# Performance work log

Measured on AMD Instinct MI355X. Metric: run time of the kernel, lower is better.

The kernel has to match this reference:

```python
import jax, jax.numpy as jnp
import numpy as np
import math

B, S, D, H = 4, 1024, 1024, 16

def setup_inputs() -> dict:
    key = jax.random.key(0)
    ks = jax.random.split(key, 9)
    Q = jax.random.normal(ks[0], (B, S, D), dtype=jnp.float32)
    K = jax.random.normal(ks[1], (B, S, D), dtype=jnp.float32)
    V = jax.random.normal(ks[2], (B, S, D), dtype=jnp.float32)
    mask = jax.random.randint(ks[3], (B, 1, S, S), 0, 2, dtype=jnp.int32)
    # keep the diagonal unmasked so no causal row is fully -inf (avoids NaN softmax rows)
    eye = jnp.eye(S, dtype=jnp.int32)[None, None]
    mask = jnp.maximum(mask, eye)
    sc = 1.0 / math.sqrt(D)
    Wq = jax.random.normal(ks[4], (D, D), dtype=jnp.float32) * sc
    Wk = jax.random.normal(ks[5], (D, D), dtype=jnp.float32) * sc
    Wv = jax.random.normal(ks[6], (D, D), dtype=jnp.float32) * sc
    Wo = jax.random.normal(ks[7], (D, D), dtype=jnp.float32) * sc
    bo = jnp.zeros((D,), dtype=jnp.float32)
    return {"Q": Q, "K": K, "V": V, "mask": mask,
            "Wq": Wq, "Wk": Wk, "Wv": Wv, "Wo": Wo, "bo": bo, "heads": H}


def reference(Q, K, V, mask, Wq, Wk, Wv, Wo, bo, heads):
    b, s, d = Q.shape
    dk = d // heads
    # QKV projections (bias-free) and head split: [B,S,D] -> [B,H,S,dk]
    def split_heads(x, W):
        return (x @ W).reshape(b, s, heads, dk).transpose(0, 2, 1, 3)
    q = split_heads(Q, Wq)
    k = split_heads(K, Wk)
    v = split_heads(V, Wv)
    # raw scores [B,H,S,S]
    attn = jnp.einsum('bhqd,bhkd->bhqk', q, k) / jnp.sqrt(jnp.float32(dk))
    # multiplicative padding mask
    attn = attn * mask.astype(attn.dtype)
    # sequential=True: torch.tril zeroes the strict upper triangle
    causal = jnp.tril(jnp.ones((s, s), dtype=attn.dtype))
    attn = attn * causal
    # the module's quirk: exact zeros become -inf before softmax
    attn = jnp.where(attn == 0, -jnp.inf, attn)
    scores = jax.nn.softmax(attn, axis=-1)  # dropout is identity in eval / p=0
    ctx = jnp.einsum('bhqk,bhkd->bhqd', scores, v)
    concat = ctx.transpose(0, 2, 1, 3).reshape(b, s, d)
    return concat @ Wo + bo
```

## Files before the change

### kernel.cpp

```cpp
#include <hip/hip_runtime.h>

#define DEV __device__ __forceinline__

typedef __bf16 bf16x8 __attribute__((ext_vector_type(8)));
typedef float f32x4 __attribute__((ext_vector_type(4)));
typedef unsigned short u16x8 __attribute__((ext_vector_type(8)));
typedef unsigned int u32;
typedef unsigned long long u64;

DEV unsigned short f2bf(float f) {
  union { float f; unsigned int u; } v; v.f = f;
  unsigned int r = v.u + 0x7fffu + ((v.u >> 16) & 1u);
  return (unsigned short)(r >> 16);
}

DEV int swz(int row, int kbyte) { return row * 128 + (kbyte ^ ((row & 7) << 4)); }

DEV void gload16(const void* g, void* l) {
  __builtin_amdgcn_global_load_lds(
      (const __attribute__((address_space(1))) unsigned int*)g,
      (__attribute__((address_space(3))) unsigned int*)l, 16, 0, 0);
}

__global__ __launch_bounds__(256) void prep_k(
    const int* __restrict__ mask, u32* __restrict__ bits,
    const float* __restrict__ Qx, const float* __restrict__ Kx, const float* __restrict__ Vx,
    unsigned short* __restrict__ qp, unsigned short* __restrict__ kp,
    unsigned short* __restrict__ vp,
    const float* __restrict__ W0, const float* __restrict__ W1,
    const float* __restrict__ W2, const float* __restrict__ W3,
    unsigned short* __restrict__ O0, unsigned short* __restrict__ O1,
    unsigned short* __restrict__ O2, unsigned short* __restrict__ O3) {
  __shared__ float tile[32][33];
  int bid = blockIdx.x, t = threadIdx.x;
  if (bid < 16384) {
    int e = bid * 256 + t;
    int k = e & 1023, q = (e >> 10) & 1023;
    int m = (mask[e] != 0) && (k <= q);
    unsigned long long b = __ballot(m);
    int lane = t & 63;
    if (lane == 0)       bits[e >> 5] = (u32)b;
    else if (lane == 32) bits[e >> 5] = (u32)(b >> 32);
  } else if (bid < 17920) {
    int r2 = bid - 16384;
    int z = r2 >> 9, tl = r2 & 511;
    const float* X = z == 0 ? Qx : z == 1 ? Kx : Vx;
    unsigned short* P = z == 0 ? qp : z == 1 ? kp : vp;
    int mb = tl >> 4, kt = tl & 15;
    size_t tb = (size_t)tl * 16384;
    #pragma unroll
    for (int i = 0; i < 4; i++) {
      int idx = i * 256 + t;
      int r = idx >> 3, j = idx & 7;
      int c0 = ((j * 16) ^ ((r & 7) << 4)) >> 1;
      const float* src = X + (size_t)(mb * 128 + r) * 1024 + kt * 64 + c0;
      f32x4 a = *(const f32x4*)src;
      f32x4 bq = *(const f32x4*)(src + 4);
      u16x8 o;
      o[0] = f2bf(a[0]); o[1] = f2bf(a[1]); o[2] = f2bf(a[2]); o[3] = f2bf(a[3]);
      o[4] = f2bf(bq[0]); o[5] = f2bf(bq[1]); o[6] = f2bf(bq[2]); o[7] = f2bf(bq[3]);
      *(u16x8*)((char*)P + tb + (size_t)idx * 16) = o;
    }
  } else {
    int r2 = bid - 17920;
    int z = r2 >> 10, rem = r2 & 1023;
    const float* W = z == 0 ? W0 : z == 1 ? W1 : z == 2 ? W2 : W3;
    unsigned short* O = z == 0 ? O0 : z == 1 ? O1 : z == 2 ? O2 : O3;
    int tx = t & 31, ty = t >> 5;
    int x0 = (rem & 31) * 32, y0 = (rem >> 5) * 32;
    #pragma unroll
    for (int i = 0; i < 4; i++)
      tile[ty + i * 8][tx] = W[(size_t)(y0 + ty + i * 8) * 1024 + x0 + tx];
    __syncthreads();
    #pragma unroll
    for (int i = 0; i < 4; i++) {
      int n = x0 + ty + i * 8, k = y0 + tx;
      size_t a = (size_t)((n >> 7) * 16 + (k >> 6)) * 16384 + swz(n & 127, (k & 63) * 2);
      *(unsigned short*)((char*)O + a) = f2bf(tile[tx][ty + i * 8]);
    }
  }
}

__global__ __launch_bounds__(256) void proj_gemm_k(
    const unsigned short* __restrict__ Qp, const unsigned short* __restrict__ Kp,
    const unsigned short* __restrict__ Vp,
    const unsigned short* __restrict__ Wtq, const unsigned short* __restrict__ Wtk,
    const unsigned short* __restrict__ Wtv,
    unsigned short* __restrict__ qo, unsigned short* __restrict__ ko,
    unsigned short* __restrict__ vo) {
  int z = blockIdx.z;
  const unsigned short* Ap = z == 0 ? Qp : z == 1 ? Kp : Vp;
  const unsigned short* Bp = z == 0 ? Wtq : z == 1 ? Wtk : Wtv;
  unsigned short* out = z == 0 ? qo : z == 1 ? ko : vo;

  __shared__ __align__(16) unsigned short As[8192];
  __shared__ __align__(16) unsigned short Bs[8192];

  int t = threadIdx.x, w = t >> 6, lane = t & 63;
  int wm = (w >> 1) * 64, wn = (w & 1) * 64;
  int rl = lane & 15, kgrp = lane >> 4;

  f32x4 acc[4][4];
  #pragma unroll
  for (int m = 0; m < 4; m++)
    #pragma unroll
    for (int n = 0; n < 4; n++)
      #pragma unroll
      for (int r = 0; r < 4; r++) acc[m][n][r] = 0.f;

  for (int kt = 0; kt < 16; kt++) {
    __syncthreads();
    const char* ab = (const char*)Ap + (size_t)(blockIdx.x * 16 + kt) * 16384 + w * 1024 + lane * 16;
    const char* bb = (const char*)Bp + (size_t)(blockIdx.y * 16 + kt) * 16384 + w * 1024 + lane * 16;
    char* al = (char*)As + w * 1024;
    char* bl = (char*)Bs + w * 1024;
    #pragma unroll
    for (int i = 0; i < 4; i++) {
      gload16(ab + i * 4096, al + i * 4096);
      gload16(bb + i * 4096, bl + i * 4096);
    }
    __syncthreads();
    #pragma unroll
    for (int kk = 0; kk < 2; kk++) {
      bf16x8 af[4], bfr[4];
      #pragma unroll
      for (int m = 0; m < 4; m++)
        af[m] = *(const bf16x8*)((const char*)As + swz(wm + m * 16 + rl, kk * 64 + kgrp * 16));
      #pragma unroll
      for (int n = 0; n < 4; n++)
        bfr[n] = *(const bf16x8*)((const char*)Bs + swz(wn + n * 16 + rl, kk * 64 + kgrp * 16));
      #pragma unroll
      for (int m = 0; m < 4; m++)
        #pragma unroll
        for (int n = 0; n < 4; n++)
          acc[m][n] = __builtin_amdgcn_mfma_f32_16x16x32_bf16(af[m], bfr[n], acc[m][n], 0, 0, 0);
    }
  }
  int m0 = blockIdx.x * 128, n0 = blockIdx.y * 128;
  #pragma unroll
  for (int m = 0; m < 4; m++)
    #pragma unroll
    for (int n = 0; n < 4; n++)
      #pragma unroll
      for (int r = 0; r < 4; r++) {
        int grow = m0 + wm + m * 16 + kgrp * 4 + r;
        int gcol = n0 + wn + n * 16 + rl;
        int b = grow >> 10, s = grow & 1023;
        int h = gcol >> 6, d = gcol & 63;
        unsigned short val = f2bf(acc[m][n][r]);
        if (z == 0) {
          out[(size_t)((b * 16 + h) * 1024 + s) * 64 + d] = val;
        } else if (z == 1) {
          *(unsigned short*)((char*)out +
            (size_t)((b * 16 + h) * 16 + (s >> 6)) * 8192 + swz(s & 63, d * 2)) = val;
        } else {
          *(unsigned short*)((char*)out +
            (size_t)((b * 16 + h) * 16 + (s >> 6)) * 8192 + swz(d, (s & 63) * 2)) = val;
        }
      }
}

__global__ __launch_bounds__(256) void attn_k(
    const unsigned short* __restrict__ qg, const unsigned short* __restrict__ kp,
    const unsigned short* __restrict__ vp, const u32* __restrict__ mbits,
    unsigned short* __restrict__ ccp) {
  int qt = 15 - (int)blockIdx.x;
  int bh = blockIdx.y;
  int b = bh >> 4, h = bh & 15;
  int t = threadIdx.x, w = t >> 6, lane = t & 63;
  int rl = lane & 15, kgrp = lane >> 4;

  const int J = qt + 1;
  const int q0 = qt * 64;

  __shared__ __align__(16) unsigned short Ks[2][4096];
  __shared__ __align__(16) unsigned short Vs[2][4096];
  __shared__ __align__(16) unsigned short Ps[4][1024];

  const size_t qoff = (size_t)bh * 65536;
  const char* kbase = (const char*)kp + (size_t)bh * 131072;
  const char* vbase = (const char*)vp + (size_t)bh * 131072;

  bf16x8 qa[2];
  {
    int row = q0 + w * 16 + rl;
    #pragma unroll
    for (int kk = 0; kk < 2; kk++)
      qa[kk] = *(const bf16x8*)(qg + qoff + (size_t)row * 64 + kk * 32 + kgrp * 8);
  }

  {
    const char* kg = kbase + w * 1024 + lane * 16;
    const char* vg = vbase + w * 1024 + lane * 16;
    char* kl = (char*)Ks[0] + w * 1024;
    char* vl = (char*)Vs[0] + w * 1024;
    gload16(kg, kl); gload16(kg + 4096, kl + 4096);
    gload16(vg, vl); gload16(vg + 4096, vl + 4096);
  }

  float lsum[4];
  f32x4 acc[4];
  #pragma unroll
  for (int r = 0; r < 4; r++) {
    lsum[r] = 0.f;
    #pragma unroll
    for (int d = 0; d < 4; d++) acc[d][r] = 0.f;
  }

  for (int j = 0; j < J; j++) {
    __syncthreads();
    if (j + 1 < J) {
      int nb = (j + 1) & 1;
      const char* kg = kbase + (size_t)(j + 1) * 8192 + w * 1024 + lane * 16;
      const char* vg = vbase + (size_t)(j + 1) * 8192 + w * 1024 + lane * 16;
      char* kl = (char*)Ks[nb] + w * 1024;
      char* vl = (char*)Vs[nb] + w * 1024;
      gload16(kg, kl); gload16(kg + 4096, kl + 4096);
      gload16(vg, vl); gload16(vg + 4096, vl + 4096);
    }
    const char* Kb = (const char*)Ks[j & 1];
    const char* Vb = (const char*)Vs[j & 1];

    f32x4 sc[4];
    #pragma unroll
    for (int n = 0; n < 4; n++) {
      f32x4 z4;
      #pragma unroll
      for (int r = 0; r < 4; r++) z4[r] = 0.f;
      bf16x8 kb0 = *(const bf16x8*)(Kb + swz(n * 16 + rl, 0 * 64 + kgrp * 16));
      bf16x8 kb1 = *(const bf16x8*)(Kb + swz(n * 16 + rl, 1 * 64 + kgrp * 16));
      z4 = __builtin_amdgcn_mfma_f32_16x16x32_bf16(qa[0], kb0, z4, 0, 0, 0);
      sc[n] = __builtin_amdgcn_mfma_f32_16x16x32_bf16(qa[1], kb1, z4, 0, 0, 0);
    }
    u32 b0[4], b1[4];
    #pragma unroll
    for (int r = 0; r < 4; r++) {
      int qrow = q0 + w * 16 + kgrp * 4 + r;
      u64 mw = *(const u64*)(mbits + ((size_t)(b * 1024 + qrow) * 32 + j * 2));
      b0[r] = (u32)mw >> rl;
      b1[r] = (u32)(mw >> 32) >> rl;
    }
    const float C = 0.18033688011112042f;
    float pe[4][4];
    #pragma unroll
    for (int n = 0; n < 4; n++) {
      #pragma unroll
      for (int r = 0; r < 4; r++) {
        u32 bit = ((n & 2) ? b1[r] : b0[r]) >> ((n & 1) << 4);
        float ex = exp2f(sc[n][r] * C);
        bool keep = (bit & 1u) && (sc[n][r] != 0.f);
        pe[n][r] = keep ? ex : 0.f;
      }
    }
    #pragma unroll
    for (int r = 0; r < 4; r++)
      lsum[r] += (pe[0][r] + pe[1][r]) + (pe[2][r] + pe[3][r]);
    unsigned short* pb = &Ps[w][0];
    #pragma unroll
    for (int n = 0; n < 4; n++) {
      int col = n * 16 + rl;
      #pragma unroll
      for (int r = 0; r < 4; r++)
        *(unsigned short*)((char*)pb + swz(kgrp * 4 + r, col * 2)) = f2bf(pe[n][r]);
    }
    bf16x8 pa[2];
    #pragma unroll
    for (int kk = 0; kk < 2; kk++)
      pa[kk] = *(const bf16x8*)((const char*)pb + swz(rl, kk * 64 + kgrp * 16));
    #pragma unroll
    for (int d = 0; d < 4; d++) {
      bf16x8 vb0 = *(const bf16x8*)(Vb + swz(d * 16 + rl, 0 * 64 + kgrp * 16));
      bf16x8 vb1 = *(const bf16x8*)(Vb + swz(d * 16 + rl, 1 * 64 + kgrp * 16));
      acc[d] = __builtin_amdgcn_mfma_f32_16x16x32_bf16(pa[0], vb0, acc[d], 0, 0, 0);
      acc[d] = __builtin_amdgcn_mfma_f32_16x16x32_bf16(pa[1], vb1, acc[d], 0, 0, 0);
    }
  }
  #pragma unroll
  for (int r = 0; r < 4; r++) {
    float l = lsum[r];
    l += __shfl_xor(l, 1); l += __shfl_xor(l, 2);
    l += __shfl_xor(l, 4); l += __shfl_xor(l, 8);
    float linv = 1.f / l;
    int srow = q0 + w * 16 + kgrp * 4 + r;
    int grow = b * 1024 + srow;
    char* tbase = (char*)ccp + (size_t)((grow >> 7) * 16 + h) * 16384;
    int rr = grow & 127;
    #pragma unroll
    for (int d = 0; d < 4; d++)
      *(unsigned short*)(tbase + swz(rr, (d * 16 + rl) * 2)) = f2bf(acc[d][r] * linv);
  }
}

__global__ __launch_bounds__(256) void out_gemm_k(
    const unsigned short* __restrict__ Ap, const unsigned short* __restrict__ Bp,
    const float* __restrict__ bias, float* __restrict__ out) {
  __shared__ __align__(16) unsigned short As[8192];
  __shared__ __align__(16) unsigned short Bs[8192];

  int t = threadIdx.x, w = t >> 6, lane = t & 63;
  int wm = (w >> 1) * 64, wn = (w & 1) * 64;
  int rl = lane & 15, kgrp = lane >> 4;

  f32x4 acc[4][4];
  #pragma unroll
  for (int m = 0; m < 4; m++)
    #pragma unroll
    for (int n = 0; n < 4; n++)
      #pragma unroll
      for (int r = 0; r < 4; r++) acc[m][n][r] = 0.f;

  for (int kt = 0; kt < 16; kt++) {
    __syncthreads();
    const char* ab = (const char*)Ap + (size_t)(blockIdx.x * 16 + kt) * 16384 + w * 1024 + lane * 16;
    const char* bb = (const char*)Bp + (size_t)(blockIdx.y * 16 + kt) * 16384 + w * 1024 + lane * 16;
    char* al = (char*)As + w * 1024;
    char* bl = (char*)Bs + w * 1024;
    #pragma unroll
    for (int i = 0; i < 4; i++) {
      gload16(ab + i * 4096, al + i * 4096);
      gload16(bb + i * 4096, bl + i * 4096);
    }
    __syncthreads();
    #pragma unroll
    for (int kk = 0; kk < 2; kk++) {
      bf16x8 af[4], bfr[4];
      #pragma unroll
      for (int m = 0; m < 4; m++)
        af[m] = *(const bf16x8*)((const char*)As + swz(wm + m * 16 + rl, kk * 64 + kgrp * 16));
      #pragma unroll
      for (int n = 0; n < 4; n++)
        bfr[n] = *(const bf16x8*)((const char*)Bs + swz(wn + n * 16 + rl, kk * 64 + kgrp * 16));
      #pragma unroll
      for (int m = 0; m < 4; m++)
        #pragma unroll
        for (int n = 0; n < 4; n++)
          acc[m][n] = __builtin_amdgcn_mfma_f32_16x16x32_bf16(af[m], bfr[n], acc[m][n], 0, 0, 0);
    }
  }
  int m0 = blockIdx.x * 128, n0 = blockIdx.y * 128;
  #pragma unroll
  for (int m = 0; m < 4; m++)
    #pragma unroll
    for (int n = 0; n < 4; n++)
      #pragma unroll
      for (int r = 0; r < 4; r++) {
        int grow = m0 + wm + m * 16 + kgrp * 4 + r;
        int gcol = n0 + wn + n * 16 + rl;
        out[(size_t)grow * 1024 + gcol] = acc[m][n][r] + bias[gcol];
      }
}

extern "C" void kernel_launch(void* const* d_in, const int* in_sizes, int n_in,
                              void* d_out, int out_size, void* d_ws, size_t ws_size,
                              hipStream_t stream) {
  const float* Q  = (const float*)d_in[0];
  const float* K  = (const float*)d_in[1];
  const float* V  = (const float*)d_in[2];
  const int* mask = (const int*)d_in[3];
  const float* Wq = (const float*)d_in[4];
  const float* Wk = (const float*)d_in[5];
  const float* Wv = (const float*)d_in[6];
  const float* Wo = (const float*)d_in[7];
  const float* bo = (const float*)d_in[8];
  float* out = (float*)d_out;

  char* ws = (char*)d_ws;
  unsigned short* xq  = (unsigned short*)(ws);
  unsigned short* xk  = (unsigned short*)(ws + (8u  << 20));
  unsigned short* xv  = (unsigned short*)(ws + (16u << 20));
  unsigned short* ccp = (unsigned short*)(ws);
  unsigned short* qb  = (unsigned short*)(ws + (24u << 20));
  unsigned short* kpk = (unsigned short*)(ws + (32u << 20));
  unsigned short* vpk = (unsigned short*)(ws + (40u << 20));
  unsigned short* wqt = (unsigned short*)(ws + (48u << 20));
  unsigned short* wkt = (unsigned short*)(ws + (50u << 20));
  unsigned short* wvt = (unsigned short*)(ws + (52u << 20));
  unsigned short* wot = (unsigned short*)(ws + (54u << 20));
  u32*            mb  = (u32*)(ws + (56u << 20));

  prep_k<<<22016, 256, 0, stream>>>(mask, mb, Q, K, V, xq, xk, xv,
                                    Wq, Wk, Wv, Wo, wqt, wkt, wvt, wot);
  proj_gemm_k<<<dim3(32, 8, 3), 256, 0, stream>>>(xq, xk, xv, wqt, wkt, wvt, qb, kpk, vpk);
  attn_k<<<dim3(16, 64), 256, 0, stream>>>(qb, kpk, vpk, mb, ccp);
  out_gemm_k<<<dim3(32, 8), 256, 0, stream>>>(ccp, wot, bo, out);
}
```

Measured before the change: 249.0 us.

## Use 128-key tiles in attention with swizzled grid and prefetched mask bits

The attention kernel now processes 128 keys per iteration instead of 64. The projection GEMM writes K and V in a matching 128-row packed, swizzled layout. Mask words are prefetched one tile ahead, MFMA sections get raised wave priority, and a 1D grid is remapped so neighbouring blocks share a batch-head across XCDs. This halves loop iterations and barriers per block. In exchange it uses more LDS and registers, and even query tiles compute a half-wasted diagonal tile.

```diff
diff --git a/kernel.cpp b/kernel.cpp
--- a/kernel.cpp
+++ b/kernel.cpp
@@ -15,6 +15,7 @@
 }
 
 DEV int swz(int row, int kbyte) { return row * 128 + (kbyte ^ ((row & 7) << 4)); }
+DEV int swzV(int row, int kbyte) { return row * 256 + (kbyte ^ ((row & 7) << 4)); }
 
 DEV void gload16(const void* g, void* l) {
   __builtin_amdgcn_global_load_lds(
@@ -152,10 +153,10 @@
           out[(size_t)((b * 16 + h) * 1024 + s) * 64 + d] = val;
         } else if (z == 1) {
           *(unsigned short*)((char*)out +
-            (size_t)((b * 16 + h) * 16 + (s >> 6)) * 8192 + swz(s & 63, d * 2)) = val;
+            (size_t)((b * 16 + h) * 8 + (s >> 7)) * 16384 + swz(s & 127, d * 2)) = val;
         } else {
           *(unsigned short*)((char*)out +
-            (size_t)((b * 16 + h) * 16 + (s >> 6)) * 8192 + swz(d, (s & 63) * 2)) = val;
+            (size_t)((b * 16 + h) * 8 + (s >> 7)) * 16384 + swzV(d, (s & 127) * 2)) = val;
         }
       }
 }
@@ -164,20 +165,21 @@
     const unsigned short* __restrict__ qg, const unsigned short* __restrict__ kp,
     const unsigned short* __restrict__ vp, const u32* __restrict__ mbits,
     unsigned short* __restrict__ ccp) {
-  int qt = 15 - (int)blockIdx.x;
-  int bh = blockIdx.y;
+  int bid = blockIdx.x;
+  int sw = (bid & 7) * 128 + (bid >> 3);
+  int bh = sw >> 4;
+  int qt = 15 - (sw & 15);
   int b = bh >> 4, h = bh & 15;
   int t = threadIdx.x, w = t >> 6, lane = t & 63;
   int rl = lane & 15, kgrp = lane >> 4;
 
-  const int J = qt + 1;
+  const int J = (qt >> 1) + 1;
   const int q0 = qt * 64;
 
-  __shared__ __align__(16) unsigned short Ks[2][4096];
-  __shared__ __align__(16) unsigned short Vs[2][4096];
-  __shared__ __align__(16) unsigned short Ps[4][1024];
-
-  const size_t qoff = (size_t)bh * 65536;
+  __shared__ __align__(16) unsigned short Ks[2][8192];
+  __shared__ __align__(16) unsigned short Vs[2][8192];
+  __shared__ __align__(16) unsigned short Ps[4][2048];
+
   const char* kbase = (const char*)kp + (size_t)bh * 131072;
   const char* vbase = (const char*)vp + (size_t)bh * 131072;
 
@@ -186,98 +188,114 @@
     int row = q0 + w * 16 + rl;
     #pragma unroll
     for (int kk = 0; kk < 2; kk++)
-      qa[kk] = *(const bf16x8*)(qg + qoff + (size_t)row * 64 + kk * 32 + kgrp * 8);
+      qa[kk] = *(const bf16x8*)(qg + (size_t)bh * 65536 + (size_t)row * 64 + kk * 32 + kgrp * 8);
   }
 
   {
-    const char* kg = kbase + w * 1024 + lane * 16;
-    const char* vg = vbase + w * 1024 + lane * 16;
-    char* kl = (char*)Ks[0] + w * 1024;
-    char* vl = (char*)Vs[0] + w * 1024;
-    gload16(kg, kl); gload16(kg + 4096, kl + 4096);
-    gload16(vg, vl); gload16(vg + 4096, vl + 4096);
-  }
-
-  float lsum[4];
+    const char* kg = kbase + w * 4096 + lane * 16;
+    const char* vg = vbase + w * 4096 + lane * 16;
+    char* kl = (char*)Ks[0] + w * 4096;
+    char* vl = (char*)Vs[0] + w * 4096;
+    #pragma unroll
+    for (int i = 0; i < 4; i++) {
+      gload16(kg + i * 1024, kl + i * 1024);
+      gload16(vg + i * 1024, vl + i * 1024);
+    }
+  }
+  u64 mcur[4][2];
+  #pragma unroll
+  for (int r = 0; r < 4; r++) {
+    int qrow = q0 + w * 16 + kgrp * 4 + r;
+    const u32* mb2 = mbits + (size_t)(b * 1024 + qrow) * 32;
+    mcur[r][0] = *(const u64*)(mb2);
+    mcur[r][1] = *(const u64*)(mb2 + 2);
+  }
+
+  float ls[4];
   f32x4 acc[4];
   #pragma unroll
   for (int r = 0; r < 4; r++) {
-    lsum[r] = 0.f;
+    ls[r] = 0.f;
     #pragma unroll
     for (int d = 0; d < 4; d++) acc[d][r] = 0.f;
   }
 
   for (int j = 0; j < J; j++) {
     __syncthreads();
+    u64 mnext[4][2] = {};
     if (j + 1 < J) {
       int nb = (j + 1) & 1;
-      const char* kg = kbase + (size_t)(j + 1) * 8192 + w * 1024 + lane * 16;
-      const char* vg = vbase + (size_t)(j + 1) * 8192 + w * 1024 + lane * 16;
-      char* kl = (char*)Ks[nb] + w * 1024;
-      char* vl = (char*)Vs[nb] + w * 1024;
-      gload16(kg, kl); gload16(kg + 4096, kl + 4096);
-      gload16(vg, vl); gload16(vg + 4096, vl + 4096);
+      const char* kg = kbase + (size_t)(j + 1) * 16384 + w * 4096 + lane * 16;
+      const char* vg = vbase + (size_t)(j + 1) * 16384 + w * 4096 + lane * 16;
+      char* kl = (char*)Ks[nb] + w * 4096;
+      char* vl = (char*)Vs[nb] + w * 4096;
+      #pragma unroll
+      for (int i = 0; i < 4; i++) {
+        gload16(kg + i * 1024, kl + i * 1024);
+        gload16(vg + i * 1024, vl + i * 1024);
+      }
+      #pragma unroll
+      for (int r = 0; r < 4; r++) {
+        int qrow = q0 + w * 16 + kgrp * 4 + r;
+        const u32* mb2 = mbits + (size_t)(b * 1024 + qrow) * 32 + (size_t)(j + 1) * 4;
+        mnext[r][0] = *(const u64*)(mb2);
+        mnext[r][1] = *(const u64*)(mb2 + 2);
+      }
     }
     const char* Kb = (const char*)Ks[j & 1];
     const char* Vb = (const char*)Vs[j & 1];
 
-    f32x4 sc[4];
-    #pragma unroll
-    for (int n = 0; n < 4; n++) {
+    f32x4 sc[8];
+    __builtin_amdgcn_s_setprio(1);
+    #pragma unroll
+    for (int n = 0; n < 8; n++) {
       f32x4 z4;
       #pragma unroll
       for (int r = 0; r < 4; r++) z4[r] = 0.f;
-      bf16x8 kb0 = *(const bf16x8*)(Kb + swz(n * 16 + rl, 0 * 64 + kgrp * 16));
-      bf16x8 kb1 = *(const bf16x8*)(Kb + swz(n * 16 + rl, 1 * 64 + kgrp * 16));
+      bf16x8 kb0 = *(const bf16x8*)(Kb + swz(n * 16 + rl, kgrp * 16));
+      bf16x8 kb1 = *(const bf16x8*)(Kb + swz(n * 16 + rl, 64 + kgrp * 16));
       z4 = __builtin_amdgcn_mfma_f32_16x16x32_bf16(qa[0], kb0, z4, 0, 0, 0);
       sc[n] = __builtin_amdgcn_mfma_f32_16x16x32_bf16(qa[1], kb1, z4, 0, 0, 0);
     }
-    u32 b0[4], b1[4];
-    #pragma unroll
-    for (int r = 0; r < 4; r++) {
-      int qrow = q0 + w * 16 + kgrp * 4 + r;
-      u64 mw = *(const u64*)(mbits + ((size_t)(b * 1024 + qrow) * 32 + j * 2));
-      b0[r] = (u32)mw >> rl;
-      b1[r] = (u32)(mw >> 32) >> rl;
-    }
+    __builtin_amdgcn_s_setprio(0);
+
+    u64 s0a[4], s1a[4];
+    #pragma unroll
+    for (int r = 0; r < 4; r++) { s0a[r] = mcur[r][0] >> rl; s1a[r] = mcur[r][1] >> rl; }
+    unsigned short* pb = &Ps[w][0];
     const float C = 0.18033688011112042f;
-    float pe[4][4];
-    #pragma unroll
-    for (int n = 0; n < 4; n++) {
+    #pragma unroll
+    for (int n = 0; n < 8; n++) {
       #pragma unroll
       for (int r = 0; r < 4; r++) {
-        u32 bit = ((n & 2) ? b1[r] : b0[r]) >> ((n & 1) << 4);
+        u32 bit = (u32)(((n < 4 ? s0a[r] : s1a[r]) >> ((n & 3) * 16)) & 1);
         float ex = exp2f(sc[n][r] * C);
-        bool keep = (bit & 1u) && (sc[n][r] != 0.f);
-        pe[n][r] = keep ? ex : 0.f;
-      }
-    }
-    #pragma unroll
-    for (int r = 0; r < 4; r++)
-      lsum[r] += (pe[0][r] + pe[1][r]) + (pe[2][r] + pe[3][r]);
-    unsigned short* pb = &Ps[w][0];
-    #pragma unroll
-    for (int n = 0; n < 4; n++) {
-      int col = n * 16 + rl;
-      #pragma unroll
-      for (int r = 0; r < 4; r++)
-        *(unsigned short*)((char*)pb + swz(kgrp * 4 + r, col * 2)) = f2bf(pe[n][r]);
-    }
-    bf16x8 pa[2];
-    #pragma unroll
-    for (int kk = 0; kk < 2; kk++)
-      pa[kk] = *(const bf16x8*)((const char*)pb + swz(rl, kk * 64 + kgrp * 16));
-    #pragma unroll
-    for (int d = 0; d < 4; d++) {
-      bf16x8 vb0 = *(const bf16x8*)(Vb + swz(d * 16 + rl, 0 * 64 + kgrp * 16));
-      bf16x8 vb1 = *(const bf16x8*)(Vb + swz(d * 16 + rl, 1 * 64 + kgrp * 16));
-      acc[d] = __builtin_amdgcn_mfma_f32_16x16x32_bf16(pa[0], vb0, acc[d], 0, 0, 0);
-      acc[d] = __builtin_amdgcn_mfma_f32_16x16x32_bf16(pa[1], vb1, acc[d], 0, 0, 0);
-    }
+        bool keep = bit && (sc[n][r] != 0.f);
+        float p = keep ? ex : 0.f;
+        ls[r] += p;
+        *(unsigned short*)((char*)pb + swzV(kgrp * 4 + r, (n * 16 + rl) * 2)) = f2bf(p);
+      }
+    }
+    bf16x8 pa[4];
+    #pragma unroll
+    for (int ks = 0; ks < 4; ks++)
+      pa[ks] = *(const bf16x8*)((const char*)pb + swzV(rl, ks * 64 + kgrp * 16));
+    __builtin_amdgcn_s_setprio(1);
+    #pragma unroll
+    for (int dd = 0; dd < 4; dd++) {
+      #pragma unroll
+      for (int ks = 0; ks < 4; ks++) {
+        bf16x8 vb = *(const bf16x8*)(Vb + swzV(dd * 16 + rl, ks * 64 + kgrp * 16));
+        acc[dd] = __builtin_amdgcn_mfma_f32_16x16x32_bf16(pa[ks], vb, acc[dd], 0, 0, 0);
+      }
+    }
+    __builtin_amdgcn_s_setprio(0);
+    #pragma unroll
+    for (int r = 0; r < 4; r++) { mcur[r][0] = mnext[r][0]; mcur[r][1] = mnext[r][1]; }
   }
   #pragma unroll
   for (int r = 0; r < 4; r++) {
-    float l = lsum[r];
+    float l = ls[r];
     l += __shfl_xor(l, 1); l += __shfl_xor(l, 2);
     l += __shfl_xor(l, 4); l += __shfl_xor(l, 8);
     float linv = 1.f / l;
@@ -381,6 +399,6 @@
   prep_k<<<22016, 256, 0, stream>>>(mask, mb, Q, K, V, xq, xk, xv,
                                     Wq, Wk, Wv, Wo, wqt, wkt, wvt, wot);
   proj_gemm_k<<<dim3(32, 8, 3), 256, 0, stream>>>(xq, xk, xv, wqt, wkt, wvt, qb, kpk, vpk);
-  attn_k<<<dim3(16, 64), 256, 0, stream>>>(qb, kpk, vpk, mb, ccp);
+  attn_k<<<1024, 256, 0, stream>>>(qb, kpk, vpk, mb, ccp);
   out_gemm_k<<<dim3(32, 8), 256, 0, stream>>>(ccp, wot, bo, out);
 }
```

Result: no change. 246.9 us (-0.8%).
